# Kernel optimization log

Measured on AMD Instinct MI355X. Metric: run time of the kernel, lower is better.

The kernel has to match this reference:

```python
import jax, jax.numpy as jnp
import numpy as np

HEAD_DIM = 128
NUM_Q_HEAD = 32
NUM_KV_HEAD = 8
GROUP_SIZE = 128
EPS = 1e-5
WINDOW = 512
CAP = 50.0
CLIP_L, CLIP_R = -0.01, 1.01
SCALE = 1.0 / np.sqrt(HEAD_DIM)
NEG = -1e9


def group_rmsnorm(x, gamma, gsz, eps):
    # x: [B, S, H]; per-group RMS over contiguous chunks of size gsz, then learned scale
    b, s, h = x.shape
    xg = x.reshape(b, s, h // gsz, gsz)
    rms = jnp.sqrt(jnp.mean(xg * xg, axis=-1, keepdims=True) + eps)
    return (xg / rms).reshape(b, s, h) * gamma


def setup_inputs() -> dict:
    key = jax.random.key(0)
    k1, k2, k3, k4, k5 = jax.random.split(key, 5)
    B, S = 2, 2048
    q = jax.random.normal(k1, (B, S, NUM_Q_HEAD, HEAD_DIM), dtype=jnp.float32)
    k = jax.random.normal(k2, (B, S, NUM_KV_HEAD, HEAD_DIM), dtype=jnp.float32)
    v = jax.random.normal(k3, (B, S, NUM_KV_HEAD, HEAD_DIM), dtype=jnp.float32)
    # GroupRMSNorm weights ~ U(init_range) = U(-1, 1)
    gamma_q = jax.random.uniform(k4, (NUM_Q_HEAD * HEAD_DIM,), dtype=jnp.float32, minval=-1.0, maxval=1.0)
    gamma_k = jax.random.uniform(k5, (NUM_KV_HEAD * HEAD_DIM,), dtype=jnp.float32, minval=-1.0, maxval=1.0)
    return {"q": q, "k": k, "v": v, "gamma_q": gamma_q, "gamma_k": gamma_k}


def reference(q, k, v, gamma_q, gamma_k):
    B, Sq, Hq, D = q.shape
    Sk, Hkv = k.shape[1], k.shape[2]
    # QK GroupRMSNorm on flattened hidden dim
    qn = group_rmsnorm(q.reshape(B, Sq, Hq * D), gamma_q, GROUP_SIZE, EPS).reshape(B, Sq, Hq, D)
    kn = group_rmsnorm(k.reshape(B, Sk, Hkv * D), gamma_k, GROUP_SIZE, EPS).reshape(B, Sk, Hkv, D)
    # GQA: repeat_interleave kv heads to match q heads
    rep = Hq // Hkv
    kr = jnp.repeat(kn, rep, axis=2)
    vr = jnp.repeat(v, rep, axis=2)
    # scores: [B, H, Sq, Sk]
    logits = jnp.einsum('bqhd,bkhd->bhqk', qn, kr) * SCALE
    # softmax capping (temperature path skipped when cap is set)
    logits = jnp.tanh(logits / CAP) * CAP
    # causal + sliding-window mask (aligned at sequence end)
    i = jnp.arange(Sq)[:, None]
    j = jnp.arange(Sk)[None, :]
    pos = i + (Sk - Sq)
    allowed = (j <= pos) & (pos - j <= WINDOW)
    logits = jnp.where(allowed, logits, NEG)
    probs = jax.nn.softmax(logits.astype(jnp.float32), axis=-1)
    # softmax clipping: clamp(probs * (r - l) + l, 0, 1)
    probs = jnp.clip(probs * (CLIP_R - CLIP_L) + CLIP_L, 0.0, 1.0)
    # output: [B, Sq, H, D]
    o = jnp.einsum('bhqk,bkhd->bqhd', probs.astype(q.dtype), vr)
    return o
```

## Files before the change

kernel.cpp:

```cpp
#include <hip/hip_runtime.h>

#define SEQ     2048
#define NQH     32
#define NKV     8
#define HD      128
#define WINDOW  512
#define QT      64
#define EPS_F   1e-5f
#define CQ2     0.12752981793f
#define PSTR    72

#define KN_OFF  0ull
#define VT_OFF  8388608ull

#define ROWPAT(r, hg) ((((r) & 3) + 8 * ((r) >> 2)) + 4 * (hg))

#define WAIT_BAR_4() asm volatile("s_waitcnt vmcnt(4)\n\ts_barrier" ::: "memory")
#define WAIT_BAR_0() asm volatile("s_waitcnt vmcnt(0)\n\ts_barrier" ::: "memory")
#define LGKM_BAR()  asm volatile("s_waitcnt lgkmcnt(0)\n\ts_barrier" ::: "memory")

using bf16x8 = __attribute__((ext_vector_type(8))) __bf16;
using f32x16 = __attribute__((ext_vector_type(16))) float;

__device__ __forceinline__ void dma16(const void* g, void* l) {
    __builtin_amdgcn_global_load_lds(
        (const __attribute__((address_space(1))) unsigned int*)g,
        (__attribute__((address_space(3))) unsigned int*)l, 16, 0, 0);
}

__global__ __launch_bounds__(256)
void prep(const float* __restrict__ k, const float* __restrict__ v,
          const float* __restrict__ gk,
          __bf16* __restrict__ kn, __bf16* __restrict__ vt)
{
    __shared__ __align__(16) __bf16 sT[HD * 72];
    const int blk = blockIdx.x;
    const int tid = threadIdx.x;
    if (blk < 512) {
        const int l16  = tid & 15;
        const int rsub = tid >> 4;
        #pragma unroll
        for (int it = 0; it < 4; it++) {
            const int row = blk * 64 + it * 16 + rsub;
            const float* src = k + (size_t)row * HD + l16 * 8;
            const float* g   = gk + (row & 7) * HD + l16 * 8;
            float4 a  = *(const float4*)(src);
            float4 b4 = *(const float4*)(src + 4);
            float ss = a.x*a.x + a.y*a.y + a.z*a.z + a.w*a.w
                     + b4.x*b4.x + b4.y*b4.y + b4.z*b4.z + b4.w*b4.w;
            ss += __shfl_xor(ss, 1); ss += __shfl_xor(ss, 2);
            ss += __shfl_xor(ss, 4); ss += __shfl_xor(ss, 8);
            const float rs = rsqrtf(ss * (1.f / 128.f) + EPS_F);
            float4 g0 = *(const float4*)(g);
            float4 g1 = *(const float4*)(g + 4);
            bf16x8 o;
            o[0] = (__bf16)(a.x  * rs * g0.x);  o[1] = (__bf16)(a.y  * rs * g0.y);
            o[2] = (__bf16)(a.z  * rs * g0.z);  o[3] = (__bf16)(a.w  * rs * g0.w);
            o[4] = (__bf16)(b4.x * rs * g1.x);  o[5] = (__bf16)(b4.y * rs * g1.y);
            o[6] = (__bf16)(b4.z * rs * g1.z);  o[7] = (__bf16)(b4.w * rs * g1.w);
            *(bf16x8*)(kn + (size_t)row * HD + l16 * 8) = o;
        }
    } else {
        const int blk2 = blk - 512;
        const int st  = blk2 & 31;
        const int kvh = (blk2 >> 5) & 7;
        const int b   = blk2 >> 8;
        const int s0  = st * 64;
        {
            const int r  = tid >> 2;
            const int q4 = tid & 3;
            const float* src = v + ((size_t)(b * SEQ + s0 + r) * NKV + kvh) * HD;
            #pragma unroll
            for (int u = 0; u < 8; u++) {
                const int d0 = q4 * 4 + u * 16;
                float4 x = *(const float4*)(src + d0);
                sT[(d0 + 0) * 72 + r] = (__bf16)x.x;
                sT[(d0 + 1) * 72 + r] = (__bf16)x.y;
                sT[(d0 + 2) * 72 + r] = (__bf16)x.z;
                sT[(d0 + 3) * 72 + r] = (__bf16)x.w;
            }
        }
        __syncthreads();
        {
            const int c     = tid & 7;
            const int dbase = tid >> 3;
            __bf16* dst = vt + ((size_t)(b * NKV + kvh) * HD) * SEQ + s0;
            #pragma unroll
            for (int i = 0; i < 4; i++) {
                const int d = dbase + i * 32;
                bf16x8 w = *(const bf16x8*)&sT[d * 72 + c * 8];
                *(bf16x8*)(dst + (size_t)d * SEQ + c * 8) = w;
            }
        }
    }
}

__global__ __launch_bounds__(256, 2)
void swa_main(const float* __restrict__ q, const __bf16* __restrict__ kn,
              const __bf16* __restrict__ vt, const float* __restrict__ gq,
              float* __restrict__ out)
{
    __shared__ __align__(16) __bf16 sKV[3][QT * HD];
    __shared__ __align__(16) __bf16 sP[QT * PSTR];
    __shared__ float sLp[2][QT];
    __shared__ float sInvL[QT];

    const int wg   = blockIdx.x;
    const int qt   = wg & 31;
    const int h    = (wg >> 5) & 31;
    const int b    = wg >> 10;
    const int kvh  = h >> 2;
    const int i0   = qt * QT;
    const int tid  = threadIdx.x;
    const int lane = tid & 63;
    const int wave = tid >> 6;
    const int mhalf = wave & 1;
    const int nhalf = wave >> 1;
    const int m    = lane & 31;
    const int hg   = lane >> 5;

    const char* k_src[4];  const char* v_src[4];
    int kq_off[4];  int v_off[4];
    {
        const char* kn_head = (const char*)kn + ((size_t)b * SEQ * NKV + kvh) * 256;
        const char* vt_head = (const char*)vt + ((size_t)(b * NKV + kvh) * HD) * (SEQ * 2);
        #pragma unroll
        for (int i = 0; i < 4; i++) {
            const int chunk = wave * 4 + i;
            {
                const int r    = chunk * 4 + (lane >> 4);
                const int cpos = lane & 15;
                const int c    = (cpos & 8) | ((cpos ^ r) & 7);
                k_src[i]  = kn_head + (size_t)r * (NKV * HD * 2) + c * 16;
                kq_off[i] = chunk * 1024;
            }
            {
                const int r    = chunk * 8 + (lane >> 3);
                const int cpos = lane & 7;
                const int c    = cpos ^ (r & 7);
                v_src[i] = vt_head + (size_t)r * (SEQ * 2) + c * 16;
                v_off[i] = chunk * 1024;
            }
        }
    }

    const int t_lo   = (i0 >= WINDOW ? (i0 - WINDOW) : 0) >> 6;
    const int t_hi   = i0 >> 6;
    const int ttbias = t_hi - 8;
    const int krow   = nhalf * 32 + m;
    const size_t kstride = (size_t)64 * (NKV * HD * 2);

    {
        const size_t ko = (size_t)t_lo * kstride;
        char* dst0 = (char*)&sKV[t_lo % 3][0];
        #pragma unroll
        for (int i = 0; i < 4; i++) dma16(k_src[i] + ko, dst0 + kq_off[i]);
        if (t_lo < t_hi) {
            char* dst1 = (char*)&sKV[(t_lo + 1) % 3][0];
            #pragma unroll
            for (int i = 0; i < 4; i++) dma16(k_src[i] + ko + kstride, dst1 + kq_off[i]);
        }
    }

    bf16x8 qf[8];
    {
        const int qrow = i0 + mhalf * 32 + m;
        const float* qp = q + ((size_t)(b * SEQ + qrow) * NQH + h) * HD;
        float4 qb[16];
        float ss = 0.0f;
        #pragma unroll
        for (int kf = 0; kf < 8; kf++) {
            const int d0 = kf * 16 + hg * 8;
            float4 a  = *(const float4*)(qp + d0);
            float4 b4 = *(const float4*)(qp + d0 + 4);
            qb[kf * 2] = a; qb[kf * 2 + 1] = b4;
            ss += a.x*a.x + a.y*a.y + a.z*a.z + a.w*a.w
                + b4.x*b4.x + b4.y*b4.y + b4.z*b4.z + b4.w*b4.w;
        }
        ss += __shfl_xor(ss, 32);
        const float rs = rsqrtf(ss * (1.f / 128.f) + EPS_F) * CQ2;
        const float* gp = gq + h * HD;
        #pragma unroll
        for (int kf = 0; kf < 8; kf++) {
            const int d0 = kf * 16 + hg * 8;
            float4 g0 = *(const float4*)(gp + d0);
            float4 g1 = *(const float4*)(gp + d0 + 4);
            bf16x8 f;
            f[0] = (__bf16)(qb[kf*2].x   * rs * g0.x);
            f[1] = (__bf16)(qb[kf*2].y   * rs * g0.y);
            f[2] = (__bf16)(qb[kf*2].z   * rs * g0.z);
            f[3] = (__bf16)(qb[kf*2].w   * rs * g0.w);
            f[4] = (__bf16)(qb[kf*2+1].x * rs * g1.x);
            f[5] = (__bf16)(qb[kf*2+1].y * rs * g1.y);
            f[6] = (__bf16)(qb[kf*2+1].z * rs * g1.z);
            f[7] = (__bf16)(qb[kf*2+1].w * rs * g1.w);
            qf[kf] = f;
        }
    }

    float lacc[16];
    #pragma unroll
    for (int i = 0; i < 16; i++) lacc[i] = 0.f;
    bf16x8 ec[9][2];

    #pragma unroll
    for (int tt = 0; tt < 9; tt++) {
        const int t = ttbias + tt;
        if (t >= t_lo) {
            if (t < t_hi) { WAIT_BAR_4(); } else { WAIT_BAR_0(); }
            const __bf16* kb = &sKV[t % 3][0];
            bf16x8 bk[8];
            #pragma unroll
            for (int kf = 0; kf < 8; kf++) {
                const int cc  = kf * 2 + hg;
                const int pos = (cc & 8) | ((cc ^ krow) & 7);
                bk[kf] = *(const bf16x8*)(kb + krow * HD + pos * 8);
            }
            if (t + 2 <= t_hi) {
                const size_t ko = (size_t)(t + 2) * kstride;
                char* dstp = (char*)&sKV[(t + 2) % 3][0];
                #pragma unroll
                for (int i = 0; i < 4; i++) dma16(k_src[i] + ko, dstp + kq_off[i]);
            }
            f32x16 c;
            #pragma unroll
            for (int i = 0; i < 16; i++) c[i] = 0.f;
            #pragma unroll
            for (int kf = 0; kf < 8; kf++)
                c = __builtin_amdgcn_mfma_f32_32x32x16_bf16(qf[kf], bk[kf], c, 0, 0, 0);

            const bool do_mask = (t == t_hi) || (t == t_lo && i0 >= WINDOW);
            const int kj = t * 64 + krow;
            float e[16];
            #pragma unroll
            for (int r = 0; r < 16; r++) {
                float ev = __builtin_amdgcn_exp2f(c[r]);
                if (do_mask) {
                    const int qi = i0 + mhalf * 32 + ROWPAT(r, hg);
                    ev = ((unsigned)(qi - kj) <= WINDOW) ? ev : 0.f;
                }
                lacc[r] += ev;
                e[r] = ev;
            }
            bf16x8 p0v, p1v;
            #pragma unroll
            for (int j = 0; j < 8; j++) { p0v[j] = (__bf16)e[j]; p1v[j] = (__bf16)e[8 + j]; }
            ec[tt][0] = p0v;  ec[tt][1] = p1v;
        }
    }

    #pragma unroll
    for (int r = 0; r < 16; r++) {
        float l = lacc[r];
        l += __shfl_xor(l, 1);  l += __shfl_xor(l, 2);  l += __shfl_xor(l, 4);
        l += __shfl_xor(l, 8);  l += __shfl_xor(l, 16);
        lacc[r] = l;
    }
    if (m == 0) {
        #pragma unroll
        for (int r = 0; r < 16; r++)
            sLp[nhalf][mhalf * 32 + ROWPAT(r, hg)] = lacc[r];
    }
    LGKM_BAR();
    {
        const size_t vo = (size_t)t_lo * 128;
        char* dst0 = (char*)&sKV[t_lo % 3][0];
        #pragma unroll
        for (int i = 0; i < 4; i++) dma16(v_src[i] + vo, dst0 + v_off[i]);
        if (t_lo < t_hi) {
            char* dst1 = (char*)&sKV[(t_lo + 1) % 3][0];
            #pragma unroll
            for (int i = 0; i < 4; i++) dma16(v_src[i] + vo + 128, dst1 + v_off[i]);
        }
    }
    if (tid < QT) sInvL[tid] = __builtin_amdgcn_rcpf(sLp[0][tid] + sLp[1][tid]);
    LGKM_BAR();

    float ar[16];
    #pragma unroll
    for (int r = 0; r < 16; r++) ar[r] = 1.02f * sInvL[mhalf * 32 + ROWPAT(r, hg)];

    f32x16 o0, o1;
    #pragma unroll
    for (int i = 0; i < 16; i++) { o0[i] = 0.f; o1[i] = 0.f; }

    #pragma unroll
    for (int tt = 0; tt < 9; tt++) {
        const int t = ttbias + tt;
        if (t >= t_lo) {
            if (t < t_hi) { WAIT_BAR_4(); } else { WAIT_BAR_0(); }
            #pragma unroll
            for (int half = 0; half < 2; half++) {
                #pragma unroll
                for (int j = 0; j < 8; j++) {
                    const int r = half * 8 + j;
                    const float ee = (float)ec[tt][half][j];
                    const float f = fminf(fmaxf(fmaf(ee, ar[r], -0.01f), 0.f), 1.f);
                    sP[(mhalf * 32 + ROWPAT(r, hg)) * PSTR + krow] = (__bf16)f;
                }
            }
            LGKM_BAR();
            const __bf16* vb = &sKV[t % 3][0];
            bf16x8 pa[4], vf0[4], vf1[4];
            #pragma unroll
            for (int kf = 0; kf < 4; kf++) {
                pa[kf] = *(const bf16x8*)&sP[(mhalf * 32 + m) * PSTR + kf * 16 + hg * 8];
                const int cc = kf * 2 + hg;
                const int row0 = nhalf * 64 + m;
                const int row1 = nhalf * 64 + 32 + m;
                vf0[kf] = *(const bf16x8*)(vb + row0 * 64 + ((cc ^ row0) & 7) * 8);
                vf1[kf] = *(const bf16x8*)(vb + row1 * 64 + ((cc ^ row1) & 7) * 8);
            }
            if (t + 2 <= t_hi) {
                const size_t vo = (size_t)(t + 2) * 128;
                char* dstp = (char*)&sKV[(t + 2) % 3][0];
                #pragma unroll
                for (int i = 0; i < 4; i++) dma16(v_src[i] + vo, dstp + v_off[i]);
            }
            #pragma unroll
            for (int kf = 0; kf < 4; kf++) {
                o0 = __builtin_amdgcn_mfma_f32_32x32x16_bf16(pa[kf], vf0[kf], o0, 0, 0, 0);
                o1 = __builtin_amdgcn_mfma_f32_32x32x16_bf16(pa[kf], vf1[kf], o1, 0, 0, 0);
            }
        }
    }

    #pragma unroll
    for (int r = 0; r < 16; r++) {
        const int row = i0 + mhalf * 32 + ROWPAT(r, hg);
        float* op = out + ((size_t)(b * SEQ + row) * NQH + h) * HD + nhalf * 64 + m;
        op[0]  = o0[r];
        op[32] = o1[r];
    }
}

extern "C" void kernel_launch(void* const* d_in, const int* in_sizes, int n_in,
                              void* d_out, int out_size, void* d_ws, size_t ws_size,
                              hipStream_t stream) {
    const float* q  = (const float*)d_in[0];
    const float* k  = (const float*)d_in[1];
    const float* v  = (const float*)d_in[2];
    const float* gq = (const float*)d_in[3];
    const float* gk = (const float*)d_in[4];
    float* out = (float*)d_out;

    __bf16* kn = (__bf16*)((char*)d_ws + KN_OFF);
    __bf16* vt = (__bf16*)((char*)d_ws + VT_OFF);

    prep<<<1024, 256, 0, stream>>>(k, v, gk, kn, vt);
    swa_main<<<2 * NQH * (SEQ / QT), 256, 0, stream>>>(q, kn, vt, gq, out);
}
```

Measured before the change: 213.1 us.

## Double-buffer P tile, remap blocks to XCDs, split QK accumulator chains

The P tile in shared memory is now double-buffered. The next tile's probabilities are written while the current tile's PV MFMAs run, which removes one barrier per iteration. Work groups are remapped so that all query heads sharing a KV head land on the same XCD, aiming for better L2 reuse of K/V. The QK MFMA chain is split into two independent accumulators, and s_setprio is raised around the MFMA blocks. The cost is extra LDS for the second P buffer and two more accumulator registers' worth of pressure, which could affect 2-block occupancy.

```diff
diff --git a/kernel.cpp b/kernel.cpp
--- a/kernel.cpp
+++ b/kernel.cpp
@@ -17,6 +17,8 @@
 
 #define WAIT_BAR_4() asm volatile("s_waitcnt vmcnt(4)\n\ts_barrier" ::: "memory")
 #define WAIT_BAR_0() asm volatile("s_waitcnt vmcnt(0)\n\ts_barrier" ::: "memory")
+#define WAIT_BARL_4() asm volatile("s_waitcnt vmcnt(4) lgkmcnt(0)\n\ts_barrier" ::: "memory")
+#define WAIT_BARL_0() asm volatile("s_waitcnt vmcnt(0) lgkmcnt(0)\n\ts_barrier" ::: "memory")
 #define LGKM_BAR()  asm volatile("s_waitcnt lgkmcnt(0)\n\ts_barrier" ::: "memory")
 
 using bf16x8 = __attribute__((ext_vector_type(8))) __bf16;
@@ -95,21 +97,38 @@
     }
 }
 
+#define WRITEP(TTW, BUF) do {                                                  \
+    _Pragma("unroll")                                                          \
+    for (int half_ = 0; half_ < 2; half_++) {                                  \
+        _Pragma("unroll")                                                      \
+        for (int j_ = 0; j_ < 8; j_++) {                                       \
+            const int r_ = half_ * 8 + j_;                                     \
+            const float ee_ = (float)ec[TTW][half_][j_];                       \
+            const float f_ = fminf(fmaxf(fmaf(ee_, ar[r_], -0.01f), 0.f), 1.f);\
+            sP[BUF][(mhalf * 32 + ROWPAT(r_, hg)) * PSTR + krow] = (__bf16)f_; \
+        }                                                                      \
+    }                                                                          \
+} while (0)
+
 __global__ __launch_bounds__(256, 2)
 void swa_main(const float* __restrict__ q, const __bf16* __restrict__ kn,
               const __bf16* __restrict__ vt, const float* __restrict__ gq,
               float* __restrict__ out)
 {
     __shared__ __align__(16) __bf16 sKV[3][QT * HD];
-    __shared__ __align__(16) __bf16 sP[QT * PSTR];
+    __shared__ __align__(16) __bf16 sP[2][QT * PSTR];
     __shared__ float sLp[2][QT];
     __shared__ float sInvL[QT];
 
-    const int wg   = blockIdx.x;
-    const int qt   = wg & 31;
-    const int h    = (wg >> 5) & 31;
-    const int b    = wg >> 10;
-    const int kvh  = h >> 2;
+    const int wg0  = blockIdx.x;
+    const int xcd  = wg0 & 7;
+    const int gi   = wg0 >> 3;
+    const int pair = xcd * 2 + (gi >> 7);
+    const int rr_  = gi & 127;
+    const int qt   = rr_ & 31;
+    const int h    = (pair & 7) * 4 + (rr_ >> 5);
+    const int b    = pair >> 3;
+    const int kvh  = pair & 7;
     const int i0   = qt * QT;
     const int tid  = threadIdx.x;
     const int lane = tid & 63;
@@ -147,6 +166,7 @@
     const int t_lo   = (i0 >= WINDOW ? (i0 - WINDOW) : 0) >> 6;
     const int t_hi   = i0 >> 6;
     const int ttbias = t_hi - 8;
+    const int tt0    = t_lo - ttbias;
     const int krow   = nhalf * 32 + m;
     const size_t kstride = (size_t)64 * (NKV * HD * 2);
 
@@ -222,19 +242,23 @@
                 #pragma unroll
                 for (int i = 0; i < 4; i++) dma16(k_src[i] + ko, dstp + kq_off[i]);
             }
-            f32x16 c;
-            #pragma unroll
-            for (int i = 0; i < 16; i++) c[i] = 0.f;
-            #pragma unroll
-            for (int kf = 0; kf < 8; kf++)
-                c = __builtin_amdgcn_mfma_f32_32x32x16_bf16(qf[kf], bk[kf], c, 0, 0, 0);
+            f32x16 c0, c1;
+            #pragma unroll
+            for (int i = 0; i < 16; i++) { c0[i] = 0.f; c1[i] = 0.f; }
+            __builtin_amdgcn_s_setprio(1);
+            #pragma unroll
+            for (int kf = 0; kf < 4; kf++) {
+                c0 = __builtin_amdgcn_mfma_f32_32x32x16_bf16(qf[2*kf],   bk[2*kf],   c0, 0, 0, 0);
+                c1 = __builtin_amdgcn_mfma_f32_32x32x16_bf16(qf[2*kf+1], bk[2*kf+1], c1, 0, 0, 0);
+            }
+            __builtin_amdgcn_s_setprio(0);
 
             const bool do_mask = (t == t_hi) || (t == t_lo && i0 >= WINDOW);
             const int kj = t * 64 + krow;
             float e[16];
             #pragma unroll
             for (int r = 0; r < 16; r++) {
-                float ev = __builtin_amdgcn_exp2f(c[r]);
+                float ev = __builtin_amdgcn_exp2f(c0[r] + c1[r]);
                 if (do_mask) {
                     const int qi = i0 + mhalf * 32 + ROWPAT(r, hg);
                     ev = ((unsigned)(qi - kj) <= WINDOW) ? ev : 0.f;
@@ -280,6 +304,9 @@
     #pragma unroll
     for (int r = 0; r < 16; r++) ar[r] = 1.02f * sInvL[mhalf * 32 + ROWPAT(r, hg)];
 
+    #pragma unroll
+    for (int tt = 0; tt < 9; tt++) if (tt == tt0) WRITEP(tt, tt & 1);
+
     f32x16 o0, o1;
     #pragma unroll
     for (int i = 0; i < 16; i++) { o0[i] = 0.f; o1[i] = 0.f; }
@@ -288,23 +315,13 @@
     for (int tt = 0; tt < 9; tt++) {
         const int t = ttbias + tt;
         if (t >= t_lo) {
-            if (t < t_hi) { WAIT_BAR_4(); } else { WAIT_BAR_0(); }
-            #pragma unroll
-            for (int half = 0; half < 2; half++) {
-                #pragma unroll
-                for (int j = 0; j < 8; j++) {
-                    const int r = half * 8 + j;
-                    const float ee = (float)ec[tt][half][j];
-                    const float f = fminf(fmaxf(fmaf(ee, ar[r], -0.01f), 0.f), 1.f);
-                    sP[(mhalf * 32 + ROWPAT(r, hg)) * PSTR + krow] = (__bf16)f;
-                }
-            }
-            LGKM_BAR();
+            if (t < t_hi) { WAIT_BARL_4(); } else { WAIT_BARL_0(); }
             const __bf16* vb = &sKV[t % 3][0];
+            const __bf16* pb = &sP[tt & 1][0];
             bf16x8 pa[4], vf0[4], vf1[4];
             #pragma unroll
             for (int kf = 0; kf < 4; kf++) {
-                pa[kf] = *(const bf16x8*)&sP[(mhalf * 32 + m) * PSTR + kf * 16 + hg * 8];
+                pa[kf] = *(const bf16x8*)&pb[(mhalf * 32 + m) * PSTR + kf * 16 + hg * 8];
                 const int cc = kf * 2 + hg;
                 const int row0 = nhalf * 64 + m;
                 const int row1 = nhalf * 64 + 32 + m;
@@ -317,11 +334,14 @@
                 #pragma unroll
                 for (int i = 0; i < 4; i++) dma16(v_src[i] + vo, dstp + v_off[i]);
             }
+            if (t + 1 <= t_hi) { WRITEP(tt + 1, (tt + 1) & 1); }
+            __builtin_amdgcn_s_setprio(1);
             #pragma unroll
             for (int kf = 0; kf < 4; kf++) {
                 o0 = __builtin_amdgcn_mfma_f32_32x32x16_bf16(pa[kf], vf0[kf], o0, 0, 0, 0);
                 o1 = __builtin_amdgcn_mfma_f32_32x32x16_bf16(pa[kf], vf1[kf], o1, 0, 0, 0);
             }
+            __builtin_amdgcn_s_setprio(0);
         }
     }
 
```

Result: no change. 215.6 us (+1.1%).
